# Performance work log

Measured on AMD Instinct MI355X. Metric: run time of the kernel, lower is better.

## Reference

```python
import jax, jax.numpy as jnp
import numpy as np

D_MODEL = 256
NUM_LAYERS = 4
NUM_FREQ = 16
D_STATE = 8
NUM_HEADS = 4
LN_EPS = 1e-5


def setup_inputs() -> dict:
    key = jax.random.key(0)
    ks = jax.random.split(key, 30)
    B, NS, NQ = 16, 1024, 1024
    D, L, S = D_MODEL, NUM_LAYERS, D_STATE
    cin = 2 * NUM_FREQ + 1  # 33
    w = lambda k, shp, s=0.02: jax.random.normal(k, shp, dtype=jnp.float32) * s
    inp = {
        'sparse_coords': jax.random.uniform(ks[0], (B, NS, 2), minval=-1.0, maxval=1.0, dtype=jnp.float32),
        'sparse_values': jax.random.normal(ks[1], (B, NS, 1), dtype=jnp.float32),
        'query_coords': jax.random.uniform(ks[2], (B, NQ, 2), minval=-1.0, maxval=1.0, dtype=jnp.float32),
        't': jax.random.uniform(ks[3], (B,), dtype=jnp.float32),
        'noise': jax.random.normal(ks[4], (B, NQ, 1), dtype=jnp.float32),
        'B_f': jax.random.normal(ks[5], (2, NUM_FREQ), dtype=jnp.float32) * 10.0,
        'Wq_in': w(ks[6], (D, cin)), 'bq_in': jnp.zeros((D,), jnp.float32),
        'Wi_in': w(ks[7], (D, cin)), 'bi_in': jnp.zeros((D,), jnp.float32),
        'A_log': jax.random.normal(ks[8], (L, S), dtype=jnp.float32) * 0.1 - 1.0,
        'Bw': w(ks[9], (L, S, D)),
        'Cw': w(ks[10], (L, D, S)),
        'Dp': jax.random.normal(ks[11], (L, D), dtype=jnp.float32) * 0.01,
        'ln_g': jnp.ones((L, D), jnp.float32), 'ln_b': jnp.zeros((L, D), jnp.float32),
        'gate_w': w(ks[12], (L, D, D)), 'gate_b': jnp.zeros((L, D), jnp.float32),
        'in_proj_w': w(ks[13], (3 * D, D)), 'in_proj_b': jnp.zeros((3 * D,), jnp.float32),
        'out_w': w(ks[14], (D, D)), 'out_b': jnp.zeros((D,), jnp.float32),
        'dec_w1': w(ks[15], (D, D)), 'dec_b1': jnp.zeros((D,), jnp.float32),
        'dec_w2': w(ks[16], (1, D)), 'dec_b2': jnp.zeros((1,), jnp.float32),
    }
    return inp


def _layernorm(x, g, b):
    mu = jnp.mean(x, axis=-1, keepdims=True)
    var = jnp.mean(jnp.square(x - mu), axis=-1, keepdims=True)
    return (x - mu) * jax.lax.rsqrt(var + LN_EPS) * g + b


def _ssm(x, A_log, Bw, Cw, Dp):
    # x: (B, N, D)
    Bsz, N, D = x.shape
    A = -jnp.clip(jnp.exp(A_log), 1e-8, 10.0)          # (S,)
    A_bar = jnp.exp(A / N)                              # dt = 1/N
    Bu = jnp.einsum('bnd,sd->bns', x, Bw)               # (B, N, S)

    def step(h, bu_t):
        h = A_bar * h + bu_t
        return h, h

    h0 = jnp.zeros((Bsz, A_log.shape[0]), x.dtype)
    _, hs = jax.lax.scan(step, h0, jnp.swapaxes(Bu, 0, 1))  # (N, B, S)
    hs = jnp.swapaxes(hs, 0, 1)                             # (B, N, S)
    return jnp.einsum('bns,ds->bnd', hs, Cw) + Dp * x


def _time_embed(t, dim):
    half = dim // 2
    freqs = jnp.exp(jnp.arange(half, dtype=jnp.float32) * (-jnp.log(10000.0) / (half - 1)))
    emb = t[:, None] * freqs[None, :]
    return jnp.concatenate([jnp.sin(emb), jnp.cos(emb)], axis=-1)


def _fourier(coords, B_f):
    proj = coords @ B_f
    return jnp.concatenate([jnp.sin(proj), jnp.cos(proj)], axis=-1)


def reference(sparse_coords, sparse_values, query_coords, t, noise, B_f,
              Wq_in, bq_in, Wi_in, bi_in,
              A_log, Bw, Cw, Dp, ln_g, ln_b, gate_w, gate_b,
              in_proj_w, in_proj_b, out_w, out_b,
              dec_w1, dec_b1, dec_w2, dec_b2):
    D = D_MODEL
    NS = sparse_coords.shape[1]
    sparse_feats = _fourier(sparse_coords, B_f)
    query_feats = _fourier(query_coords, B_f)
    input_tokens = jnp.concatenate([sparse_feats, sparse_values], -1) @ Wi_in.T + bi_in
    query_tokens = jnp.concatenate([query_feats, noise], -1) @ Wq_in.T + bq_in
    t_emb = _time_embed(t, D)[:, None, :]
    seq = jnp.concatenate([input_tokens + t_emb, query_tokens + t_emb], axis=1)

    for l in range(A_log.shape[0]):
        xn = _layernorm(seq, ln_g[l], ln_b[l])
        gate = jax.nn.sigmoid(xn @ gate_w[l].T + gate_b[l])
        seq = seq + gate * _ssm(xn, A_log[l], Bw[l], Cw[l], Dp[l])

    input_seq = seq[:, :NS, :]
    query_seq = seq[:, NS:, :]

    # multi-head cross-attention (torch nn.MultiheadAttention semantics)
    H, hd = NUM_HEADS, D // NUM_HEADS
    q = query_seq @ in_proj_w[:D].T + in_proj_b[:D]
    k = input_seq @ in_proj_w[D:2 * D].T + in_proj_b[D:2 * D]
    v = input_seq @ in_proj_w[2 * D:].T + in_proj_b[2 * D:]
    def split(x):
        b, n, _ = x.shape
        return x.reshape(b, n, H, hd).transpose(0, 2, 1, 3)
    q, k, v = split(q), split(k), split(v)
    scores = jnp.einsum('bhqd,bhkd->bhqk', q, k) / jnp.sqrt(jnp.float32(hd))
    attn = jax.nn.softmax(scores, axis=-1)
    o = jnp.einsum('bhqk,bhkd->bhqd', attn, v)
    o = o.transpose(0, 2, 1, 3).reshape(query_seq.shape[0], -1, D)
    attended = o @ out_w.T + out_b

    h = jax.nn.relu(attended @ dec_w1.T + dec_b1)
    return h @ dec_w2.T + dec_b2
```

## Files before the change

kernel.cpp:

```cpp
#include <hip/hip_runtime.h>
#include <math.h>


typedef float floatx4 __attribute__((ext_vector_type(4)));
typedef short shortx8 __attribute__((ext_vector_type(8)));

__device__ __forceinline__ unsigned short f2bf(float f) {
  unsigned u = __builtin_bit_cast(unsigned, f);
  u += 0x7FFFu + ((u >> 16) & 1u);
  return (unsigned short)(u >> 16);
}
__device__ __forceinline__ float bf2f(unsigned short h) {
  unsigned u = ((unsigned)h) << 16;
  return __builtin_bit_cast(float, u);
}
__device__ __forceinline__ unsigned cvt_pk_bf16(float a, float b) {
  unsigned r;
  asm("v_cvt_pk_bf16_f32 %0, %1, %2" : "=v"(r) : "v"(a), "v"(b));
  return r;
}
__device__ __forceinline__ void split2(float f0, float f1, unsigned& ph, unsigned& pl) {
  ph = cvt_pk_bf16(f0, f1);
  float r0 = f0 - __builtin_bit_cast(float, ph << 16);
  float r1 = f1 - __builtin_bit_cast(float, ph & 0xFFFF0000u);
  pl = cvt_pk_bf16(r0, r1);
}
__device__ __forceinline__ void split8(float4 a, float4 b, uint4& uh, uint4& ul) {
  unsigned h0, h1, h2, h3, l0, l1, l2, l3;
  split2(a.x, a.y, h0, l0);
  split2(a.z, a.w, h1, l1);
  split2(b.x, b.y, h2, l2);
  split2(b.z, b.w, h3, l3);
  uh = make_uint4(h0, h1, h2, h3);
  ul = make_uint4(l0, l1, l2, l3);
}
__device__ __forceinline__ shortx8 lds_frag(const unsigned short* S, int row, int u) {
  uint4 v = *(const uint4*)(S + row * 64 + ((u ^ (row & 7)) << 3));
  return __builtin_bit_cast(shortx8, v);
}
__device__ __forceinline__ shortx8 lds_frag_v(const unsigned short* S, int row, int u) {
  uint4 v = *(const uint4*)(S + row * 64 + (((u ^ row ^ (row >> 3)) & 7) << 3));
  return __builtin_bit_cast(shortx8, v);
}
__device__ __forceinline__ shortx8 gfrag(const unsigned short* p) {
  return __builtin_bit_cast(shortx8, *(const uint4*)p);
}
__device__ __forceinline__ floatx4 mfma16(shortx8 a, shortx8 b, floatx4 c) {
  return __builtin_amdgcn_mfma_f32_16x16x32_bf16(a, b, c, 0, 0, 0);
}
__device__ __forceinline__ float wave_sum64(float v) {
#pragma unroll
  for (int m = 1; m < 64; m <<= 1) v += __shfl_xor(v, m);
  return v;
}

__global__ __launch_bounds__(256) void wconv_k(
    const float* __restrict__ gw, const float* __restrict__ ipw,
    const float* __restrict__ ow, const float* __restrict__ d1w,
    unsigned short* __restrict__ dh, unsigned short* __restrict__ dl) {
  int i = (blockIdx.x * 256 + threadIdx.x) * 8;
  const float* src;
  if (i < 262144) src = gw + i;
  else if (i < 458752) src = ipw + (i - 262144);
  else if (i < 524288) src = ow + (i - 458752);
  else src = d1w + (i - 524288);
  uint4 uh, ul;
  split8(*(const float4*)src, *(const float4*)(src + 4), uh, ul);
  *(uint4*)(dh + i) = uh;
  *(uint4*)(dl + i) = ul;
}

__global__ __launch_bounds__(256) void wconv2_k(
    const float* __restrict__ Wi, const float* __restrict__ Wq,
    unsigned short* __restrict__ eh, unsigned short* __restrict__ el) {
  int idx = blockIdx.x * 256 + threadIdx.x;
  int sel = idx >> 14, rem = idx & 16383;
  int row = rem >> 6, k = rem & 63;
  float v = 0.f;
  if (k < 33) v = (sel ? Wq : Wi)[row * 33 + k];
  unsigned short h = f2bf(v);
  eh[idx] = h;
  el[idx] = f2bf(v - bf2f(h));
}

__global__ __launch_bounds__(256) void embed_k(
    const float* __restrict__ sc, const float* __restrict__ sv,
    const float* __restrict__ qc, const float* __restrict__ tarr,
    const float* __restrict__ noise, const float* __restrict__ Bf,
    const float* __restrict__ bq, const float* __restrict__ bi,
    const unsigned short* __restrict__ Weh, const unsigned short* __restrict__ Wel,
    float* __restrict__ seq) {
  __shared__ unsigned short Ah[64 * 64];
  __shared__ unsigned short Al[64 * 64];
  __shared__ float teb[256];
  int tid = threadIdx.x;
  int bid = blockIdx.x;
  int chunk = bid & 15, half = (bid >> 4) & 1, b = bid >> 5;
  int rowbase = b * 2048 + half * 1024 + chunk * 64;
  {
    uint4 z = make_uint4(0, 0, 0, 0);
    *(uint4*)(Ah + tid * 8) = z;
    *(uint4*)(Ah + 2048 + tid * 8) = z;
    *(uint4*)(Al + tid * 8) = z;
    *(uint4*)(Al + 2048 + tid * 8) = z;
  }
  {
    float t = tarr[b];
    int dd = tid & 127;
    float e = t * __expf((float)dd * -0.07252236513367074f);
    float v = (tid < 128) ? sinf(e) : cosf(e);
    teb[tid] = v + (half ? bq : bi)[tid];
  }
  __syncthreads();
  {
    int tok = tid >> 2;
    int n = chunk * 64 + tok;
    const float* cp = (half ? qc : sc) + (size_t)(b * 1024 + n) * 2;
    float cx = cp[0], cy = cp[1];
#pragma unroll
    for (int jj = 0; jj < 4; ++jj) {
      int fr = (tid & 3) * 4 + jj;
      float px = cx * Bf[fr] + cy * Bf[16 + fr];
      float s = sinf(px), c = cosf(px);
      unsigned short sh = f2bf(s), ch = f2bf(c);
      int ks = fr, kc = 16 + fr;
      Ah[tok * 64 + (((ks >> 3) ^ (tok & 7)) << 3) + (ks & 7)] = sh;
      Al[tok * 64 + (((ks >> 3) ^ (tok & 7)) << 3) + (ks & 7)] = f2bf(s - bf2f(sh));
      Ah[tok * 64 + (((kc >> 3) ^ (tok & 7)) << 3) + (kc & 7)] = ch;
      Al[tok * 64 + (((kc >> 3) ^ (tok & 7)) << 3) + (kc & 7)] = f2bf(c - bf2f(ch));
    }
    if ((tid & 3) == 0) {
      float vv = (half ? noise : sv)[b * 1024 + n];
      unsigned short vh = f2bf(vv);
      Ah[tok * 64 + ((4 ^ (tok & 7)) << 3)] = vh;
      Al[tok * 64 + ((4 ^ (tok & 7)) << 3)] = f2bf(vv - bf2f(vh));
    }
  }
  __syncthreads();
  int w = tid >> 6, lane = tid & 63, lm = lane & 15, quad = lane >> 4;
  const unsigned short* Wb = Weh + half * 16384;
  const unsigned short* Wbl = Wel + half * 16384;
  floatx4 acc[4][4] = {};
#pragma unroll
  for (int s = 0; s < 2; ++s) {
    shortx8 afh[4], afl[4];
#pragma unroll
    for (int i = 0; i < 4; ++i) {
      afh[i] = lds_frag(Ah, i * 16 + lm, s * 4 + quad);
      afl[i] = lds_frag(Al, i * 16 + lm, s * 4 + quad);
    }
#pragma unroll
    for (int n = 0; n < 4; ++n) {
      int wr = w * 64 + n * 16 + lm;
      shortx8 bh = gfrag(Wb + wr * 64 + (s * 4 + quad) * 8);
      shortx8 bl = gfrag(Wbl + wr * 64 + (s * 4 + quad) * 8);
#pragma unroll
      for (int i = 0; i < 4; ++i) {
        acc[i][n] = mfma16(afl[i], bh, acc[i][n]);
        acc[i][n] = mfma16(afh[i], bl, acc[i][n]);
        acc[i][n] = mfma16(afh[i], bh, acc[i][n]);
      }
    }
  }
#pragma unroll
  for (int i = 0; i < 4; ++i)
#pragma unroll
    for (int n = 0; n < 4; ++n) {
      int col = w * 64 + n * 16 + lm;
      float te = teb[col];
#pragma unroll
      for (int r = 0; r < 4; ++r) {
        int tok = i * 16 + quad * 4 + r;
        seq[(size_t)(rowbase + tok) * 256 + col] = acc[i][n][r] + te;
      }
    }
}

__global__ __launch_bounds__(256) void scan_k(
    const float* __restrict__ BuT, const float* __restrict__ A_log,
    float* __restrict__ hsT) {
  int tid = threadIdx.x;
  int wid = blockIdx.x * 4 + (tid >> 6);
  int lane = tid & 63;
  int b = wid >> 3, s = wid & 7;
  float A = -fminf(fmaxf(expf(A_log[s]), 1e-8f), 10.0f);
  float abar = expf(A * (1.0f / 2048.0f));
  size_t base = (size_t)s * 32768 + b * 2048 + lane * 32;
  const float4* bu4 = (const float4*)(BuT + base);
  float4 v[8];
#pragma unroll
  for (int k = 0; k < 8; ++k) v[k] = bu4[k];
  float bl = 0.f;
#pragma unroll
  for (int k = 0; k < 8; ++k) {
    bl = abar * bl + v[k].x;
    bl = abar * bl + v[k].y;
    bl = abar * bl + v[k].z;
    bl = abar * bl + v[k].w;
  }
  float a = expf(A * (32.0f / 2048.0f));
  float bb = bl;
#pragma unroll
  for (int off = 1; off < 64; off <<= 1) {
    float pa = __shfl_up(a, (unsigned)off);
    float pb = __shfl_up(bb, (unsigned)off);
    if (lane >= off) { bb = a * pb + bb; a = a * pa; }
  }
  float h = __shfl_up(bb, 1u);
  if (lane == 0) h = 0.f;
  float4* hp4 = (float4*)(hsT + base);
#pragma unroll
  for (int k = 0; k < 8; ++k) {
    float h0 = abar * h + v[k].x;
    float h1 = abar * h0 + v[k].y;
    float h2 = abar * h1 + v[k].z;
    float h3 = abar * h2 + v[k].w;
    hp4[k] = make_float4(h0, h1, h2, h3);
    h = h3;
  }
}

template <int HASUPD>
__global__ __launch_bounds__(256, 2) void pe_k(
    float* __restrict__ seq, const float* __restrict__ Gprev,
    const float* __restrict__ hsTp, const float* __restrict__ CwP,
    const float* __restrict__ DpP, const float* __restrict__ gP,
    const float* __restrict__ bP, const float* __restrict__ gC,
    const float* __restrict__ bC, const float* __restrict__ BwL,
    const unsigned short* __restrict__ Wh, const unsigned short* __restrict__ Wl,
    const float* __restrict__ gbias, float* __restrict__ Gout,
    float* __restrict__ BuT) {
  __shared__ unsigned short slab[64 * 536];
  __shared__ float hsL[8 * 64];
  __shared__ float BwLds[8 * 256];
  int tid = threadIdx.x;
  int m0 = (int)blockIdx.x * 64;
  int w = tid >> 6, lane = tid & 63, lm = lane & 15, quad = lane >> 4;

#pragma unroll
  for (int j = 0; j < 8; ++j) BwLds[j * 256 + tid] = BwL[j * 256 + tid];
  if (HASUPD) {
    hsL[tid] = hsTp[(size_t)(tid >> 6) * 32768 + m0 + (tid & 63)];
    int v1 = tid + 256;
    hsL[v1] = hsTp[(size_t)(v1 >> 6) * 32768 + m0 + (v1 & 63)];
  }

  if (HASUPD) {
    __syncthreads();
    int c0 = lane * 4;
    float cw[4][8], dp4[4];
#pragma unroll
    for (int n = 0; n < 4; ++n) {
      float4 a0 = *(const float4*)(CwP + (size_t)(c0 + n) * 8);
      float4 a1 = *(const float4*)(CwP + (size_t)(c0 + n) * 8 + 4);
      cw[n][0] = a0.x; cw[n][1] = a0.y; cw[n][2] = a0.z; cw[n][3] = a0.w;
      cw[n][4] = a1.x; cw[n][5] = a1.y; cw[n][6] = a1.z; cw[n][7] = a1.w;
      dp4[n] = DpP[c0 + n];
    }
    float4 gg = *(const float4*)(gP + c0);
    float4 bb = *(const float4*)(bP + c0);
#pragma unroll
    for (int rr = 0; rr < 16; ++rr) {
      int r = w * 16 + rr;
      int row = m0 + r;
      float4 x = *(const float4*)(seq + (size_t)row * 256 + c0);
      float s1 = x.x + x.y + x.z + x.w;
      float s2 = x.x * x.x + x.y * x.y + x.z * x.z + x.w * x.w;
#pragma unroll
      for (int mk = 1; mk < 64; mk <<= 1) {
        s1 += __shfl_xor(s1, mk);
        s2 += __shfl_xor(s2, mk);
      }
      float mu = s1 * (1.0f / 256.0f);
      float var = s2 * (1.0f / 256.0f) - mu * mu;
      float rs = rsqrtf(var + 1e-5f);
      float xn0 = (x.x - mu) * rs * gg.x + bb.x;
      float xn1 = (x.y - mu) * rs * gg.y + bb.y;
      float xn2 = (x.z - mu) * rs * gg.z + bb.z;
      float xn3 = (x.w - mu) * rs * gg.w + bb.w;
      float hv[8];
#pragma unroll
      for (int s = 0; s < 8; ++s) hv[s] = hsL[s * 64 + r];
      float y0 = dp4[0] * xn0, y1 = dp4[1] * xn1, y2 = dp4[2] * xn2, y3 = dp4[3] * xn3;
#pragma unroll
      for (int s = 0; s < 8; ++s) {
        y0 += hv[s] * cw[0][s];
        y1 += hv[s] * cw[1][s];
        y2 += hv[s] * cw[2][s];
        y3 += hv[s] * cw[3][s];
      }
      float4 gp = *(const float4*)(Gprev + (size_t)row * 256 + c0);
      x.x += gp.x * y0; x.y += gp.y * y1; x.z += gp.z * y2; x.w += gp.w * y3;
      *(float4*)(seq + (size_t)row * 256 + c0) = x;
      *(float4*)((char*)slab + (size_t)r * 1072 + c0 * 4) = x;
    }
    __syncthreads();
  }

  {
    int r = tid >> 2, q2 = tid & 3;
    int row = m0 + r;
    float4 xr[16];
#pragma unroll
    for (int j = 0; j < 16; ++j) {
      if (HASUPD)
        xr[j] = *(const float4*)((const char*)slab + (size_t)r * 1072 + (q2 * 64 + j * 4) * 4);
      else
        xr[j] = *(const float4*)(seq + (size_t)row * 256 + q2 * 64 + j * 4);
    }
    __syncthreads();
    float s1 = 0.f, s2 = 0.f;
#pragma unroll
    for (int j = 0; j < 16; ++j) {
      s1 += (xr[j].x + xr[j].y) + (xr[j].z + xr[j].w);
      s2 += (xr[j].x * xr[j].x + xr[j].y * xr[j].y) + (xr[j].z * xr[j].z + xr[j].w * xr[j].w);
    }
    s1 += __shfl_xor(s1, 1); s2 += __shfl_xor(s2, 1);
    s1 += __shfl_xor(s1, 2); s2 += __shfl_xor(s2, 2);
    float mu = s1 * (1.0f / 256.0f);
    float var = s2 * (1.0f / 256.0f) - mu * mu;
    float rs = rsqrtf(var + 1e-5f);
    float bu[8] = {};
#pragma unroll
    for (int j = 0; j < 16; ++j) {
      int c = q2 * 64 + j * 4;
      float4 gg = *(const float4*)(gC + c);
      float4 bb = *(const float4*)(bC + c);
      float4 xn;
      xn.x = (xr[j].x - mu) * rs * gg.x + bb.x;
      xn.y = (xr[j].y - mu) * rs * gg.y + bb.y;
      xn.z = (xr[j].z - mu) * rs * gg.z + bb.z;
      xn.w = (xr[j].w - mu) * rs * gg.w + bb.w;
#pragma unroll
      for (int s = 0; s < 8; ++s) {
        const float4 bw = *(const float4*)(BwLds + s * 256 + c);
        bu[s] += (xn.x * bw.x + xn.y * bw.y) + (xn.z * bw.z + xn.w * bw.w);
      }
      unsigned h0, l0, h1, l1;
      split2(xn.x, xn.y, h0, l0);
      split2(xn.z, xn.w, h1, l1);
      *(uint2*)((char*)slab + (size_t)r * 1072 + c * 2) = make_uint2(h0, h1);
      *(uint2*)((char*)slab + (size_t)r * 1072 + 512 + c * 2) = make_uint2(l0, l1);
    }
#pragma unroll
    for (int s = 0; s < 8; ++s) {
      bu[s] += __shfl_xor(bu[s], 1);
      bu[s] += __shfl_xor(bu[s], 2);
    }
    if (q2 == 0) {
#pragma unroll
      for (int s = 0; s < 8; ++s) BuT[(size_t)s * 32768 + row] = bu[s];
    }
  }
  __syncthreads();

  floatx4 acc[4][4] = {};
  {
    uint4 wa[8], wb[8];
    const size_t wcbase = (size_t)(w * 64 + lm) * 256 + quad * 8;
#pragma unroll
    for (int n = 0; n < 4; ++n) {
      wa[n * 2]     = *(const uint4*)(Wh + wcbase + (size_t)n * 16 * 256);
      wa[n * 2 + 1] = *(const uint4*)(Wl + wcbase + (size_t)n * 16 * 256);
    }
#pragma unroll
    for (int ku = 0; ku < 8; ++ku) {
      uint4* cur = (ku & 1) ? wb : wa;
      uint4* nxt = (ku & 1) ? wa : wb;
      if (ku < 7) {
        size_t koff = wcbase + (size_t)(ku + 1) * 32;
#pragma unroll
        for (int n = 0; n < 4; ++n) {
          nxt[n * 2]     = *(const uint4*)(Wh + koff + (size_t)n * 16 * 256);
          nxt[n * 2 + 1] = *(const uint4*)(Wl + koff + (size_t)n * 16 * 256);
        }
      }
      int slot = ku * 4 + quad;
      shortx8 afh[4], afl[4];
#pragma unroll
      for (int m = 0; m < 4; ++m) {
        const char* rb = (const char*)slab + (size_t)(m * 16 + lm) * 1072;
        afh[m] = __builtin_bit_cast(shortx8, *(const uint4*)(rb + slot * 16));
        afl[m] = __builtin_bit_cast(shortx8, *(const uint4*)(rb + 512 + slot * 16));
      }
#pragma unroll
      for (int m = 0; m < 4; ++m)
#pragma unroll
        for (int n = 0; n < 4; ++n) {
          shortx8 bh = __builtin_bit_cast(shortx8, cur[n * 2]);
          shortx8 bl = __builtin_bit_cast(shortx8, cur[n * 2 + 1]);
          acc[m][n] = mfma16(afl[m], bh, acc[m][n]);
          acc[m][n] = mfma16(afh[m], bl, acc[m][n]);
          acc[m][n] = mfma16(afh[m], bh, acc[m][n]);
        }
    }
  }
  float bi4[4];
#pragma unroll
  for (int n = 0; n < 4; ++n) bi4[n] = gbias[w * 64 + n * 16 + lm];
#pragma unroll
  for (int m = 0; m < 4; ++m)
#pragma unroll
    for (int r = 0; r < 4; ++r) {
      int row = m0 + m * 16 + quad * 4 + r;
#pragma unroll
      for (int n = 0; n < 4; ++n) {
        int col = w * 64 + n * 16 + lm;
        float v = acc[m][n][r] + bi4[n];
        Gout[(size_t)row * 256 + col] = 1.0f / (1.0f + __expf(-v));
      }
    }
}

__global__ __launch_bounds__(256) void upd_k(
    float* __restrict__ seq, const float* __restrict__ G,
    const float* __restrict__ hsT, const float* __restrict__ Cw,
    const float* __restrict__ Dp, const float* __restrict__ g,
    const float* __restrict__ be) {
  int tid = threadIdx.x;
  int row = blockIdx.x * 4 + (tid >> 6);
  int lane = tid & 63;
  int c0 = lane * 4;
  float4 x = *(const float4*)(seq + (size_t)row * 256 + c0);
  float s1 = x.x + x.y + x.z + x.w;
  float s2 = x.x * x.x + x.y * x.y + x.z * x.z + x.w * x.w;
#pragma unroll
  for (int mk = 1; mk < 64; mk <<= 1) {
    s1 += __shfl_xor(s1, mk);
    s2 += __shfl_xor(s2, mk);
  }
  float mu = s1 * (1.0f / 256.0f);
  float var = s2 * (1.0f / 256.0f) - mu * mu;
  float rs = rsqrtf(var + 1e-5f);
  float4 gg = *(const float4*)(g + c0);
  float4 bb = *(const float4*)(be + c0);
  float xn0 = (x.x - mu) * rs * gg.x + bb.x;
  float xn1 = (x.y - mu) * rs * gg.y + bb.y;
  float xn2 = (x.z - mu) * rs * gg.z + bb.z;
  float xn3 = (x.w - mu) * rs * gg.w + bb.w;
  float hv[8];
#pragma unroll
  for (int s = 0; s < 8; ++s) hv[s] = hsT[(size_t)s * 32768 + row];
  float y0, y1, y2, y3;
  {
    float4 d = *(const float4*)(Dp + c0);
    y0 = d.x * xn0; y1 = d.y * xn1; y2 = d.z * xn2; y3 = d.w * xn3;
  }
#pragma unroll
  for (int n = 0; n < 4; ++n) {
    float4 a0 = *(const float4*)(Cw + (size_t)(c0 + n) * 8);
    float4 a1 = *(const float4*)(Cw + (size_t)(c0 + n) * 8 + 4);
    float yn = hv[0] * a0.x + hv[1] * a0.y + hv[2] * a0.z + hv[3] * a0.w +
               hv[4] * a1.x + hv[5] * a1.y + hv[6] * a1.z + hv[7] * a1.w;
    if (n == 0) y0 += yn;
    else if (n == 1) y1 += yn;
    else if (n == 2) y2 += yn;
    else y3 += yn;
  }
  float4 gp = *(const float4*)(G + (size_t)row * 256 + c0);
  x.x += gp.x * y0; x.y += gp.y * y1; x.z += gp.z * y2; x.w += gp.w * y3;
  *(float4*)(seq + (size_t)row * 256 + c0) = x;
}

template <int MODE, int ASPLIT>
__global__ __launch_bounds__(256, 4) void mgemm_k(
    const void* __restrict__ Aptr, const unsigned short* __restrict__ Alp,
    const unsigned short* __restrict__ Wh, const unsigned short* __restrict__ Wl,
    const float* __restrict__ bias, void* __restrict__ C0, void* __restrict__ C1,
    int ldc, int aClog, int aStride, int aBase, int gxlog) {
  __shared__ unsigned short Ash[64 * 64];
  __shared__ unsigned short Asl[64 * 64];
  __shared__ unsigned short Bsh[64 * 72];
  __shared__ unsigned short Bsl[64 * 72];
  int tid = threadIdx.x;
  int nwg = (int)gridDim.x;
  int vbid = ((blockIdx.x & 7) * (nwg >> 3)) + (blockIdx.x >> 3);
  int bx = vbid & ((1 << gxlog) - 1);
  int by = vbid >> gxlog;
  int n0 = bx * 64, m0 = by * 64;
  int w = tid >> 6, lane = tid & 63;
  int wm = w & 1, wn = w >> 1;
  int lm = lane & 15, quad = lane >> 4;
  int sr2 = tid >> 2, q2 = tid & 3;
  unsigned aMask = (1u << aClog) - 1u;
  int am = m0 + sr2;
  int garow = ((am >> aClog) * aStride) + aBase + (int)((unsigned)am & aMask);
  int wrow = n0 + sr2;
  uint4 ah[2], al[2], wh4[2], wl4[2];
  auto load_chunk = [&](int kc) {
    if (ASPLIT) {
      const unsigned short* pa =
          (const unsigned short*)Aptr + (size_t)garow * 256 + kc * 64 + q2 * 8;
      ah[0] = *(const uint4*)pa;
      ah[1] = *(const uint4*)(pa + 32);
      const unsigned short* pl = Alp + (pa - (const unsigned short*)Aptr);
      al[0] = *(const uint4*)pl;
      al[1] = *(const uint4*)(pl + 32);
    } else {
      const float* pa = (const float*)Aptr + (size_t)garow * 256 + kc * 64 + q2 * 8;
      split8(*(const float4*)pa, *(const float4*)(pa + 4), ah[0], al[0]);
      split8(*(const float4*)(pa + 32), *(const float4*)(pa + 36), ah[1], al[1]);
    }
    const unsigned short* pw = Wh + (size_t)wrow * 256 + kc * 64 + q2 * 8;
    wh4[0] = *(const uint4*)pw;
    wh4[1] = *(const uint4*)(pw + 32);
    const unsigned short* pwl = Wl + (pw - Wh);
    wl4[0] = *(const uint4*)pwl;
    wl4[1] = *(const uint4*)(pwl + 32);
  };
  int kc0 = (bx + 1) & 3;
  load_chunk(kc0);
  floatx4 acc[2][2] = {};
  for (int j = 0; j < 4; ++j) {
    __syncthreads();
    {
      int off0 = sr2 * 64 + ((q2 ^ (sr2 & 7)) << 3);
      int off1 = sr2 * 64 + (((q2 + 4) ^ (sr2 & 7)) << 3);
      *(uint4*)(Ash + off0) = ah[0];
      *(uint4*)(Ash + off1) = ah[1];
      *(uint4*)(Asl + off0) = al[0];
      *(uint4*)(Asl + off1) = al[1];
      *(uint4*)(Bsh + off0) = wh4[0];
      *(uint4*)(Bsh + off1) = wh4[1];
      *(uint4*)(Bsl + off0) = wl4[0];
      *(uint4*)(Bsl + off1) = wl4[1];
    }
    __syncthreads();
    if (j < 3) load_chunk((kc0 + j + 1) & 3);
#pragma unroll
    for (int s = 0; s < 2; ++s) {
      int u = s * 4 + quad;
      shortx8 afh[2], afl[2], bfh[2], bfl[2];
#pragma unroll
      for (int i = 0; i < 2; ++i) {
        int rr = wm * 32 + i * 16 + lm;
        afh[i] = lds_frag(Ash, rr, u);
        afl[i] = lds_frag(Asl, rr, u);
        int rc = wn * 32 + i * 16 + lm;
        bfh[i] = lds_frag(Bsh, rc, u);
        bfl[i] = lds_frag(Bsl, rc, u);
      }
#pragma unroll
      for (int i = 0; i < 2; ++i)
#pragma unroll
        for (int n = 0; n < 2; ++n) {
          acc[i][n] = mfma16(afl[i], bfh[n], acc[i][n]);
          acc[i][n] = mfma16(afh[i], bfl[n], acc[i][n]);
          acc[i][n] = mfma16(afh[i], bfh[n], acc[i][n]);
        }
    }
  }
  if (MODE == 3) {
    unsigned short* Ch = (unsigned short*)C0;
    unsigned short* Cl = (unsigned short*)C1;
    float bi4[2];
#pragma unroll
    for (int n = 0; n < 2; ++n) bi4[n] = bias[n0 + wn * 32 + n * 16 + lm];
    __syncthreads();
#pragma unroll
    for (int i = 0; i < 2; ++i)
#pragma unroll
      for (int r = 0; r < 4; ++r) {
        int rr = wm * 32 + i * 16 + quad * 4 + r;
        int c0i = wn * 32 + lm;
        float vA = acc[i][0][r] + bi4[0];
        float vB = acc[i][1][r] + bi4[1];
        unsigned ph, pl;
        split2(vA, vB, ph, pl);
        Bsh[rr * 72 + c0i] = (unsigned short)ph;
        Bsh[rr * 72 + c0i + 16] = (unsigned short)(ph >> 16);
        Bsl[rr * 72 + c0i] = (unsigned short)pl;
        Bsl[rr * 72 + c0i + 16] = (unsigned short)(pl >> 16);
      }
    __syncthreads();
#pragma unroll
    for (int f = 0; f < 2; ++f) {
      int row = (tid >> 3) + f * 32;
      int slot = tid & 7;
      size_t go = (size_t)(m0 + row) * ldc + n0 + slot * 8;
      *(uint4*)(Ch + go) = *(const uint4*)(Bsh + row * 72 + slot * 8);
      *(uint4*)(Cl + go) = *(const uint4*)(Bsl + row * 72 + slot * 8);
    }
  } else {
    float* Cf = (float*)C0;
#pragma unroll
    for (int i = 0; i < 2; ++i)
#pragma unroll
      for (int r = 0; r < 4; ++r) {
        int row = m0 + wm * 32 + i * 16 + quad * 4 + r;
#pragma unroll
        for (int n = 0; n < 2; ++n) {
          int col = n0 + wn * 32 + n * 16 + lm;
          float v = acc[i][n][r] + bias[col];
          if (MODE == 1) v = fmaxf(v, 0.0f);
          Cf[(size_t)row * ldc + col] = v;
        }
      }
  }
}

__global__ __launch_bounds__(256, 2) void attn_k(
    const unsigned short* __restrict__ qh, const unsigned short* __restrict__ ql,
    const unsigned short* __restrict__ kvh, const unsigned short* __restrict__ kvl,
    float* __restrict__ ob) {
  __shared__ unsigned short Ksh[2][64 * 64];
  __shared__ unsigned short Ksl[2][64 * 64];
  __shared__ unsigned short Vt[2][64 * 64];
  __shared__ unsigned short Ps[4 * 16 * 64];
  int tid = threadIdx.x;
  int bid = blockIdx.x;
  int bh = bid & 63, qt = bid >> 6;
  int h = bh & 3, b = bh >> 2;
  int w = tid >> 6, lane = tid & 63, lm = lane & 15, quad = lane >> 4;
  int sr = tid >> 3, scu = tid & 7;
  unsigned short* Pw = Ps + w * 1024;
  shortx8 qfh[2], qfl[2];
  {
    size_t qoff = (size_t)(b * 1024 + qt * 64 + w * 16 + lm) * 256 + h * 64;
#pragma unroll
    for (int s = 0; s < 2; ++s) {
      qfh[s] = gfrag(qh + qoff + s * 32 + quad * 8);
      qfl[s] = gfrag(ql + qoff + s * 32 + quad * 8);
    }
  }
  float lac = 0.f;
  floatx4 oacc[4] = {};
  const size_t kvbase = ((size_t)(b * 1024)) * 512 + h * 64;
  const float sc_l2 = 0.125f * 1.44269504089f;
  int vg = tid & 7, vk = (tid >> 3) * 2;
  uint4 kh4[2], kl4[2], vv0, vv1;
  auto load_kv = [&](int kt) {
#pragma unroll
    for (int p = 0; p < 2; ++p) {
      int r = sr + p * 32;
      size_t a = kvbase + (size_t)(kt * 64 + r) * 512 + scu * 8;
      kh4[p] = *(const uint4*)(kvh + a);
      kl4[p] = *(const uint4*)(kvl + a);
    }
    vv0 = *(const uint4*)(kvh + kvbase + (size_t)(kt * 64 + vk) * 512 + 256 + vg * 8);
    vv1 = *(const uint4*)(kvh + kvbase + (size_t)(kt * 64 + vk + 1) * 512 + 256 + vg * 8);
  };
  const int kt0 = qt & 15;
  load_kv(kt0);
  for (int it = 0; it < 16; ++it) {
    int cur = it & 1;
    unsigned short* KshC = Ksh[cur];
    unsigned short* KslC = Ksl[cur];
    unsigned short* VtC = Vt[cur];
#pragma unroll
    for (int p = 0; p < 2; ++p) {
      int r = sr + p * 32;
      int off = r * 64 + ((scu ^ (r & 7)) << 3);
      *(uint4*)(KshC + off) = kh4[p];
      *(uint4*)(KslC + off) = kl4[p];
    }
    {
      shortx8 s0 = __builtin_bit_cast(shortx8, vv0);
      shortx8 s1 = __builtin_bit_cast(shortx8, vv1);
      unsigned short* vb = VtC + vg * 512 + (vk & 7);
      int x0 = ((vk >> 3) ^ vg) & 7;
#pragma unroll
      for (int j = 0; j < 8; ++j) {
        unsigned pack = ((unsigned)(unsigned short)s0[j]) |
                        (((unsigned)(unsigned short)s1[j]) << 16);
        *(unsigned*)(vb + j * 64 + ((x0 ^ j) << 3)) = pack;
      }
    }
    __syncthreads();
    if (it < 15) load_kv((kt0 + it + 1) & 15);
    floatx4 sacc[4] = {};
#pragma unroll
    for (int s = 0; s < 2; ++s) {
#pragma unroll
      for (int m = 0; m < 4; ++m) {
        shortx8 kfh = lds_frag(KshC, m * 16 + lm, s * 4 + quad);
        shortx8 kfl = lds_frag(KslC, m * 16 + lm, s * 4 + quad);
        sacc[m] = mfma16(kfl, qfh[s], sacc[m]);
        sacc[m] = mfma16(kfh, qfl[s], sacc[m]);
        sacc[m] = mfma16(kfh, qfh[s], sacc[m]);
      }
    }
#pragma unroll
    for (int m = 0; m < 4; ++m) {
      float p0 = exp2f(sacc[m][0] * sc_l2 - 12.0f);
      float p1 = exp2f(sacc[m][1] * sc_l2 - 12.0f);
      float p2 = exp2f(sacc[m][2] * sc_l2 - 12.0f);
      float p3 = exp2f(sacc[m][3] * sc_l2 - 12.0f);
      lac += (p0 + p1) + (p2 + p3);
      int u = (m * 2 + (quad >> 1)) ^ (lm & 7);
      unsigned short* base = Pw + lm * 64 + u * 8 + (quad & 1) * 4;
      *(uint2*)base = make_uint2(cvt_pk_bf16(p0, p1), cvt_pk_bf16(p2, p3));
    }
#pragma unroll
    for (int s = 0; s < 2; ++s) {
      shortx8 pf = lds_frag(Pw, lm, s * 4 + quad);
#pragma unroll
      for (int n = 0; n < 4; ++n) {
        shortx8 vf = lds_frag_v(VtC, n * 16 + lm, s * 4 + quad);
        oacc[n] = mfma16(pf, vf, oacc[n]);
      }
    }
  }
  lac += __shfl_xor(lac, 16);
  lac += __shfl_xor(lac, 32);
  const size_t obase = ((size_t)(b * 1024 + qt * 64 + w * 16)) * 256 + h * 64;
#pragma unroll
  for (int r = 0; r < 4; ++r) {
    int row = quad * 4 + r;
    float inv = 1.0f / __shfl(lac, row);
#pragma unroll
    for (int n = 0; n < 4; ++n)
      ob[obase + (size_t)row * 256 + n * 16 + lm] = oacc[n][r] * inv;
  }
}

__global__ __launch_bounds__(256) void dec2_k(const float* __restrict__ hb,
                                              const float* __restrict__ w2,
                                              const float* __restrict__ b2,
                                              float* __restrict__ out) {
  int tid = threadIdx.x;
  int m = blockIdx.x * 4 + (tid >> 6);
  int lane = tid & 63;
  float4 h4 = *(const float4*)(hb + (size_t)m * 256 + lane * 4);
  float4 w4 = *(const float4*)(w2 + lane * 4);
  float v = h4.x * w4.x + h4.y * w4.y + h4.z * w4.z + h4.w * w4.w;
  v = wave_sum64(v);
  if (lane == 0) out[m] = v + b2[0];
}

extern "C" void kernel_launch(void* const* d_in, const int* in_sizes, int n_in,
                              void* d_out, int out_size, void* d_ws, size_t ws_size,
                              hipStream_t stream) {
  const float* sparse_coords = (const float*)d_in[0];
  const float* sparse_values = (const float*)d_in[1];
  const float* query_coords  = (const float*)d_in[2];
  const float* t_arr         = (const float*)d_in[3];
  const float* noise         = (const float*)d_in[4];
  const float* B_f           = (const float*)d_in[5];
  const float* Wq_in         = (const float*)d_in[6];
  const float* bq_in         = (const float*)d_in[7];
  const float* Wi_in         = (const float*)d_in[8];
  const float* bi_in         = (const float*)d_in[9];
  const float* A_log         = (const float*)d_in[10];
  const float* Bw            = (const float*)d_in[11];
  const float* Cw            = (const float*)d_in[12];
  const float* Dp            = (const float*)d_in[13];
  const float* ln_g          = (const float*)d_in[14];
  const float* ln_b          = (const float*)d_in[15];
  const float* gate_w        = (const float*)d_in[16];
  const float* gate_b        = (const float*)d_in[17];
  const float* in_proj_w     = (const float*)d_in[18];
  const float* in_proj_b     = (const float*)d_in[19];
  const float* out_w         = (const float*)d_in[20];
  const float* out_b         = (const float*)d_in[21];
  const float* dec_w1        = (const float*)d_in[22];
  const float* dec_b1        = (const float*)d_in[23];
  const float* dec_w2        = (const float*)d_in[24];
  const float* dec_b2        = (const float*)d_in[25];

  unsigned short* us = (unsigned short*)d_ws;
  float* seq = (float*)us;
  float* G = (float*)(us + 16777216);
  unsigned short* qhp = us + 33554432;
  unsigned short* qlp = qhp + 4194304;
  unsigned short* kvh = qlp + 4194304;
  unsigned short* kvl = kvh + 8388608;
  float* BuT = (float*)(kvl + 8388608);
  float* hsT = BuT + 262144;
  unsigned short* whi = (unsigned short*)(hsT + 262144);
  unsigned short* wlo = whi + 589824;
  unsigned short* Weh = wlo + 589824;
  unsigned short* Wel = Weh + 32768;
  float* obuf = G;
  float* attb = (float*)qhp;
  float* hrel = (float*)kvh;

  wconv_k<<<288, 256, 0, stream>>>(gate_w, in_proj_w, out_w, dec_w1, whi, wlo);
  wconv2_k<<<128, 256, 0, stream>>>(Wi_in, Wq_in, Weh, Wel);
  embed_k<<<512, 256, 0, stream>>>(sparse_coords, sparse_values, query_coords,
                                   t_arr, noise, B_f, bq_in, bi_in, Weh, Wel, seq);
  pe_k<0><<<512, 256, 0, stream>>>(seq, nullptr, nullptr, nullptr, nullptr,
                                   nullptr, nullptr, ln_g, ln_b, Bw,
                                   whi, wlo, gate_b, G, BuT);
  scan_k<<<32, 256, 0, stream>>>(BuT, A_log, hsT);
  for (int l = 1; l < 4; ++l) {
    pe_k<1><<<512, 256, 0, stream>>>(
        seq, G, hsT, Cw + (l - 1) * 2048, Dp + (l - 1) * 256,
        ln_g + (l - 1) * 256, ln_b + (l - 1) * 256,
        ln_g + l * 256, ln_b + l * 256, Bw + l * 2048,
        whi + l * 65536, wlo + l * 65536, gate_b + l * 256, G, BuT);
    scan_k<<<32, 256, 0, stream>>>(BuT, A_log + l * 8, hsT);
  }
  upd_k<<<8192, 256, 0, stream>>>(seq, G, hsT, Cw + 3 * 2048, Dp + 3 * 256,
                                  ln_g + 768, ln_b + 768);
  mgemm_k<3, 0><<<1024, 256, 0, stream>>>(
      seq, nullptr, whi + 262144, wlo + 262144, in_proj_b, qhp, qlp,
      256, 10, 2048, 1024, 2);
  mgemm_k<3, 0><<<2048, 256, 0, stream>>>(
      seq, nullptr, whi + 327680, wlo + 327680, in_proj_b + 256, kvh, kvl,
      512, 10, 2048, 0, 3);
  attn_k<<<1024, 256, 0, stream>>>(qhp, qlp, kvh, kvl, obuf);
  mgemm_k<0, 0><<<1024, 256, 0, stream>>>(
      obuf, nullptr, whi + 458752, wlo + 458752, out_b, attb, nullptr,
      256, 30, 0, 0, 2);
  mgemm_k<1, 0><<<1024, 256, 0, stream>>>(
      attb, nullptr, whi + 524288, wlo + 524288, dec_b1, hrel, nullptr,
      256, 30, 0, 0, 2);
  dec2_k<<<4096, 256, 0, stream>>>(hrel, dec_w2, dec_b2, (float*)d_out);
}
```

Measured before the change: 543.0 us.

## Restructure projection GEMMs as row-slab kernels and fuse decoder chain

Replaces the tiled 64x64 split-bf16 GEMM with row-slab kernels. Each block splits a 32-row fp32 slab into hi/lo bf16 in LDS once, and each wave streams its weight columns straight from global memory with register double-buffering, so there is no per-k-chunk LDS staging of weights. The out-projection, first decoder layer with ReLU and final dot product are fused into one kernel, keeping intermediates in LDS and dropping two intermediate global round-trips and two launches. The cost is fewer, larger blocks at lower occupancy and weights re-read from global/L2 by every block.

```diff
diff --git a/kernel.cpp b/kernel.cpp
--- a/kernel.cpp
+++ b/kernel.cpp
@@ -462,141 +462,266 @@
   *(float4*)(seq + (size_t)row * 256 + c0) = x;
 }
 
-template <int MODE, int ASPLIT>
-__global__ __launch_bounds__(256, 4) void mgemm_k(
-    const void* __restrict__ Aptr, const unsigned short* __restrict__ Alp,
-    const unsigned short* __restrict__ Wh, const unsigned short* __restrict__ Wl,
-    const float* __restrict__ bias, void* __restrict__ C0, void* __restrict__ C1,
-    int ldc, int aClog, int aStride, int aBase, int gxlog) {
-  __shared__ unsigned short Ash[64 * 64];
-  __shared__ unsigned short Asl[64 * 64];
-  __shared__ unsigned short Bsh[64 * 72];
-  __shared__ unsigned short Bsl[64 * 72];
+template <int NPASS>
+__global__ __launch_bounds__(256, 2) void proj_k(
+    const float* __restrict__ src, const unsigned short* __restrict__ Wh,
+    const unsigned short* __restrict__ Wl, const float* __restrict__ bias,
+    unsigned short* __restrict__ Ch, unsigned short* __restrict__ Cl,
+    int ldc, int aBase) {
+  __shared__ unsigned short slab[32 * 536];
   int tid = threadIdx.x;
-  int nwg = (int)gridDim.x;
-  int vbid = ((blockIdx.x & 7) * (nwg >> 3)) + (blockIdx.x >> 3);
-  int bx = vbid & ((1 << gxlog) - 1);
-  int by = vbid >> gxlog;
-  int n0 = bx * 64, m0 = by * 64;
-  int w = tid >> 6, lane = tid & 63;
-  int wm = w & 1, wn = w >> 1;
-  int lm = lane & 15, quad = lane >> 4;
-  int sr2 = tid >> 2, q2 = tid & 3;
-  unsigned aMask = (1u << aClog) - 1u;
-  int am = m0 + sr2;
-  int garow = ((am >> aClog) * aStride) + aBase + (int)((unsigned)am & aMask);
-  int wrow = n0 + sr2;
-  uint4 ah[2], al[2], wh4[2], wl4[2];
-  auto load_chunk = [&](int kc) {
-    if (ASPLIT) {
-      const unsigned short* pa =
-          (const unsigned short*)Aptr + (size_t)garow * 256 + kc * 64 + q2 * 8;
-      ah[0] = *(const uint4*)pa;
-      ah[1] = *(const uint4*)(pa + 32);
-      const unsigned short* pl = Alp + (pa - (const unsigned short*)Aptr);
-      al[0] = *(const uint4*)pl;
-      al[1] = *(const uint4*)(pl + 32);
-    } else {
-      const float* pa = (const float*)Aptr + (size_t)garow * 256 + kc * 64 + q2 * 8;
-      split8(*(const float4*)pa, *(const float4*)(pa + 4), ah[0], al[0]);
-      split8(*(const float4*)(pa + 32), *(const float4*)(pa + 36), ah[1], al[1]);
-    }
-    const unsigned short* pw = Wh + (size_t)wrow * 256 + kc * 64 + q2 * 8;
-    wh4[0] = *(const uint4*)pw;
-    wh4[1] = *(const uint4*)(pw + 32);
-    const unsigned short* pwl = Wl + (pw - Wh);
-    wl4[0] = *(const uint4*)pwl;
-    wl4[1] = *(const uint4*)(pwl + 32);
-  };
-  int kc0 = (bx + 1) & 3;
-  load_chunk(kc0);
-  floatx4 acc[2][2] = {};
-  for (int j = 0; j < 4; ++j) {
-    __syncthreads();
+  int m0 = (int)blockIdx.x * 32;
+  int w = tid >> 6, lane = tid & 63, lm = lane & 15, quad = lane >> 4;
+  {
+    int r = tid >> 3, q8 = tid & 7;
+    int am = m0 + r;
+    int garow = ((am >> 10) * 2048) + aBase + (am & 1023);
+    const float* sp = src + (size_t)garow * 256 + q8 * 32;
+    char* rb = (char*)slab + (size_t)r * 1072;
+#pragma unroll
+    for (int j = 0; j < 8; ++j) {
+      float4 x = *(const float4*)(sp + j * 4);
+      unsigned h0, l0, h1, l1;
+      split2(x.x, x.y, h0, l0);
+      split2(x.z, x.w, h1, l1);
+      int c = q8 * 32 + j * 4;
+      *(uint2*)(rb + c * 2) = make_uint2(h0, h1);
+      *(uint2*)(rb + 512 + c * 2) = make_uint2(l0, l1);
+    }
+  }
+  __syncthreads();
+#pragma unroll
+  for (int cp = 0; cp < NPASS; ++cp) {
+    floatx4 acc[2][4] = {};
     {
-      int off0 = sr2 * 64 + ((q2 ^ (sr2 & 7)) << 3);
-      int off1 = sr2 * 64 + (((q2 + 4) ^ (sr2 & 7)) << 3);
-      *(uint4*)(Ash + off0) = ah[0];
-      *(uint4*)(Ash + off1) = ah[1];
-      *(uint4*)(Asl + off0) = al[0];
-      *(uint4*)(Asl + off1) = al[1];
-      *(uint4*)(Bsh + off0) = wh4[0];
-      *(uint4*)(Bsh + off1) = wh4[1];
-      *(uint4*)(Bsl + off0) = wl4[0];
-      *(uint4*)(Bsl + off1) = wl4[1];
-    }
-    __syncthreads();
-    if (j < 3) load_chunk((kc0 + j + 1) & 3);
-#pragma unroll
-    for (int s = 0; s < 2; ++s) {
-      int u = s * 4 + quad;
-      shortx8 afh[2], afl[2], bfh[2], bfl[2];
-#pragma unroll
-      for (int i = 0; i < 2; ++i) {
-        int rr = wm * 32 + i * 16 + lm;
-        afh[i] = lds_frag(Ash, rr, u);
-        afl[i] = lds_frag(Asl, rr, u);
-        int rc = wn * 32 + i * 16 + lm;
-        bfh[i] = lds_frag(Bsh, rc, u);
-        bfl[i] = lds_frag(Bsl, rc, u);
-      }
-#pragma unroll
-      for (int i = 0; i < 2; ++i)
-#pragma unroll
-        for (int n = 0; n < 2; ++n) {
-          acc[i][n] = mfma16(afl[i], bfh[n], acc[i][n]);
-          acc[i][n] = mfma16(afh[i], bfl[n], acc[i][n]);
-          acc[i][n] = mfma16(afh[i], bfh[n], acc[i][n]);
-        }
-    }
-  }
-  if (MODE == 3) {
-    unsigned short* Ch = (unsigned short*)C0;
-    unsigned short* Cl = (unsigned short*)C1;
-    float bi4[2];
-#pragma unroll
-    for (int n = 0; n < 2; ++n) bi4[n] = bias[n0 + wn * 32 + n * 16 + lm];
-    __syncthreads();
-#pragma unroll
-    for (int i = 0; i < 2; ++i)
+      uint4 wa[8], wb[8];
+      const size_t wcbase = (size_t)(cp * 256 + w * 64 + lm) * 256 + quad * 8;
+#pragma unroll
+      for (int n = 0; n < 4; ++n) {
+        wa[n * 2]     = *(const uint4*)(Wh + wcbase + (size_t)n * 16 * 256);
+        wa[n * 2 + 1] = *(const uint4*)(Wl + wcbase + (size_t)n * 16 * 256);
+      }
+#pragma unroll
+      for (int ku = 0; ku < 8; ++ku) {
+        uint4* cur = (ku & 1) ? wb : wa;
+        uint4* nxt = (ku & 1) ? wa : wb;
+        if (ku < 7) {
+          size_t koff = wcbase + (size_t)(ku + 1) * 32;
+#pragma unroll
+          for (int n = 0; n < 4; ++n) {
+            nxt[n * 2]     = *(const uint4*)(Wh + koff + (size_t)n * 16 * 256);
+            nxt[n * 2 + 1] = *(const uint4*)(Wl + koff + (size_t)n * 16 * 256);
+          }
+        }
+        int slot = ku * 4 + quad;
+        shortx8 afh[2], afl[2];
+#pragma unroll
+        for (int m = 0; m < 2; ++m) {
+          const char* rb = (const char*)slab + (size_t)(m * 16 + lm) * 1072;
+          afh[m] = __builtin_bit_cast(shortx8, *(const uint4*)(rb + slot * 16));
+          afl[m] = __builtin_bit_cast(shortx8, *(const uint4*)(rb + 512 + slot * 16));
+        }
+#pragma unroll
+        for (int m = 0; m < 2; ++m)
+#pragma unroll
+          for (int n = 0; n < 4; ++n) {
+            shortx8 bh = __builtin_bit_cast(shortx8, cur[n * 2]);
+            shortx8 bl = __builtin_bit_cast(shortx8, cur[n * 2 + 1]);
+            acc[m][n] = mfma16(afl[m], bh, acc[m][n]);
+            acc[m][n] = mfma16(afh[m], bl, acc[m][n]);
+            acc[m][n] = mfma16(afh[m], bh, acc[m][n]);
+          }
+      }
+    }
+    float bi4[4];
+#pragma unroll
+    for (int n = 0; n < 4; ++n) bi4[n] = bias[cp * 256 + w * 64 + n * 16 + lm];
+#pragma unroll
+    for (int m = 0; m < 2; ++m)
 #pragma unroll
       for (int r = 0; r < 4; ++r) {
-        int rr = wm * 32 + i * 16 + quad * 4 + r;
-        int c0i = wn * 32 + lm;
-        float vA = acc[i][0][r] + bi4[0];
-        float vB = acc[i][1][r] + bi4[1];
-        unsigned ph, pl;
-        split2(vA, vB, ph, pl);
-        Bsh[rr * 72 + c0i] = (unsigned short)ph;
-        Bsh[rr * 72 + c0i + 16] = (unsigned short)(ph >> 16);
-        Bsl[rr * 72 + c0i] = (unsigned short)pl;
-        Bsl[rr * 72 + c0i + 16] = (unsigned short)(pl >> 16);
-      }
-    __syncthreads();
-#pragma unroll
-    for (int f = 0; f < 2; ++f) {
-      int row = (tid >> 3) + f * 32;
-      int slot = tid & 7;
-      size_t go = (size_t)(m0 + row) * ldc + n0 + slot * 8;
-      *(uint4*)(Ch + go) = *(const uint4*)(Bsh + row * 72 + slot * 8);
-      *(uint4*)(Cl + go) = *(const uint4*)(Bsl + row * 72 + slot * 8);
-    }
-  } else {
-    float* Cf = (float*)C0;
-#pragma unroll
-    for (int i = 0; i < 2; ++i)
+        int row = m0 + m * 16 + quad * 4 + r;
+        size_t ro = (size_t)row * ldc + cp * 256;
+#pragma unroll
+        for (int np = 0; np < 2; ++np) {
+          int colA = w * 64 + (2 * np) * 16 + lm;
+          float vA = acc[m][2 * np][r] + bi4[2 * np];
+          float vB = acc[m][2 * np + 1][r] + bi4[2 * np + 1];
+          unsigned ph, pl;
+          split2(vA, vB, ph, pl);
+          Ch[ro + colA] = (unsigned short)ph;
+          Ch[ro + colA + 16] = (unsigned short)(ph >> 16);
+          Cl[ro + colA] = (unsigned short)pl;
+          Cl[ro + colA + 16] = (unsigned short)(pl >> 16);
+        }
+      }
+  }
+}
+
+__global__ __launch_bounds__(256, 2) void dec_k(
+    const float* __restrict__ src, const unsigned short* __restrict__ W1h,
+    const unsigned short* __restrict__ W1l, const float* __restrict__ b1,
+    const unsigned short* __restrict__ W2h, const unsigned short* __restrict__ W2l,
+    const float* __restrict__ b2v, const float* __restrict__ w2,
+    const float* __restrict__ b2, float* __restrict__ out) {
+  __shared__ unsigned short slab[32 * 536];
+  __shared__ float pw[4][32];
+  int tid = threadIdx.x;
+  int m0 = (int)blockIdx.x * 32;
+  int w = tid >> 6, lane = tid & 63, lm = lane & 15, quad = lane >> 4;
+  {
+    int r = tid >> 3, q8 = tid & 7;
+    const float* sp = src + (size_t)(m0 + r) * 256 + q8 * 32;
+    char* rb = (char*)slab + (size_t)r * 1072;
+#pragma unroll
+    for (int j = 0; j < 8; ++j) {
+      float4 x = *(const float4*)(sp + j * 4);
+      unsigned h0, l0, h1, l1;
+      split2(x.x, x.y, h0, l0);
+      split2(x.z, x.w, h1, l1);
+      int c = q8 * 32 + j * 4;
+      *(uint2*)(rb + c * 2) = make_uint2(h0, h1);
+      *(uint2*)(rb + 512 + c * 2) = make_uint2(l0, l1);
+    }
+  }
+  __syncthreads();
+  floatx4 acc[2][4] = {};
+  {
+    uint4 wa[8], wb[8];
+    const size_t wcbase = (size_t)(w * 64 + lm) * 256 + quad * 8;
+#pragma unroll
+    for (int n = 0; n < 4; ++n) {
+      wa[n * 2]     = *(const uint4*)(W1h + wcbase + (size_t)n * 16 * 256);
+      wa[n * 2 + 1] = *(const uint4*)(W1l + wcbase + (size_t)n * 16 * 256);
+    }
+#pragma unroll
+    for (int ku = 0; ku < 8; ++ku) {
+      uint4* cur = (ku & 1) ? wb : wa;
+      uint4* nxt = (ku & 1) ? wa : wb;
+      if (ku < 7) {
+        size_t koff = wcbase + (size_t)(ku + 1) * 32;
+#pragma unroll
+        for (int n = 0; n < 4; ++n) {
+          nxt[n * 2]     = *(const uint4*)(W1h + koff + (size_t)n * 16 * 256);
+          nxt[n * 2 + 1] = *(const uint4*)(W1l + koff + (size_t)n * 16 * 256);
+        }
+      }
+      int slot = ku * 4 + quad;
+      shortx8 afh[2], afl[2];
+#pragma unroll
+      for (int m = 0; m < 2; ++m) {
+        const char* rb = (const char*)slab + (size_t)(m * 16 + lm) * 1072;
+        afh[m] = __builtin_bit_cast(shortx8, *(const uint4*)(rb + slot * 16));
+        afl[m] = __builtin_bit_cast(shortx8, *(const uint4*)(rb + 512 + slot * 16));
+      }
+#pragma unroll
+      for (int m = 0; m < 2; ++m)
+#pragma unroll
+        for (int n = 0; n < 4; ++n) {
+          shortx8 bh = __builtin_bit_cast(shortx8, cur[n * 2]);
+          shortx8 bl = __builtin_bit_cast(shortx8, cur[n * 2 + 1]);
+          acc[m][n] = mfma16(afl[m], bh, acc[m][n]);
+          acc[m][n] = mfma16(afh[m], bl, acc[m][n]);
+          acc[m][n] = mfma16(afh[m], bh, acc[m][n]);
+        }
+    }
+  }
+  __syncthreads();
+  {
+    float bi4[4];
+#pragma unroll
+    for (int n = 0; n < 4; ++n) bi4[n] = b1[w * 64 + n * 16 + lm];
+#pragma unroll
+    for (int m = 0; m < 2; ++m)
 #pragma unroll
       for (int r = 0; r < 4; ++r) {
-        int row = m0 + wm * 32 + i * 16 + quad * 4 + r;
-#pragma unroll
-        for (int n = 0; n < 2; ++n) {
-          int col = n0 + wn * 32 + n * 16 + lm;
-          float v = acc[i][n][r] + bias[col];
-          if (MODE == 1) v = fmaxf(v, 0.0f);
-          Cf[(size_t)row * ldc + col] = v;
-        }
-      }
-  }
+        int rr = m * 16 + quad * 4 + r;
+        char* rb = (char*)slab + (size_t)rr * 1072;
+#pragma unroll
+        for (int np = 0; np < 2; ++np) {
+          int cA = w * 64 + (2 * np) * 16 + lm;
+          int cB = cA + 16;
+          float vA = acc[m][2 * np][r] + bi4[2 * np];
+          float vB = acc[m][2 * np + 1][r] + bi4[2 * np + 1];
+          unsigned ph, pl;
+          split2(vA, vB, ph, pl);
+          *(unsigned short*)(rb + cA * 2) = (unsigned short)ph;
+          *(unsigned short*)(rb + cB * 2) = (unsigned short)(ph >> 16);
+          *(unsigned short*)(rb + 512 + cA * 2) = (unsigned short)pl;
+          *(unsigned short*)(rb + 512 + cB * 2) = (unsigned short)(pl >> 16);
+        }
+      }
+  }
+  __syncthreads();
+  floatx4 acc2[2][4] = {};
+  {
+    uint4 wa[8], wb[8];
+    const size_t wcbase = (size_t)(w * 64 + lm) * 256 + quad * 8;
+#pragma unroll
+    for (int n = 0; n < 4; ++n) {
+      wa[n * 2]     = *(const uint4*)(W2h + wcbase + (size_t)n * 16 * 256);
+      wa[n * 2 + 1] = *(const uint4*)(W2l + wcbase + (size_t)n * 16 * 256);
+    }
+#pragma unroll
+    for (int ku = 0; ku < 8; ++ku) {
+      uint4* cur = (ku & 1) ? wb : wa;
+      uint4* nxt = (ku & 1) ? wa : wb;
+      if (ku < 7) {
+        size_t koff = wcbase + (size_t)(ku + 1) * 32;
+#pragma unroll
+        for (int n = 0; n < 4; ++n) {
+          nxt[n * 2]     = *(const uint4*)(W2h + koff + (size_t)n * 16 * 256);
+          nxt[n * 2 + 1] = *(const uint4*)(W2l + koff + (size_t)n * 16 * 256);
+        }
+      }
+      int slot = ku * 4 + quad;
+      shortx8 afh[2], afl[2];
+#pragma unroll
+      for (int m = 0; m < 2; ++m) {
+        const char* rb = (const char*)slab + (size_t)(m * 16 + lm) * 1072;
+        afh[m] = __builtin_bit_cast(shortx8, *(const uint4*)(rb + slot * 16));
+        afl[m] = __builtin_bit_cast(shortx8, *(const uint4*)(rb + 512 + slot * 16));
+      }
+#pragma unroll
+      for (int m = 0; m < 2; ++m)
+#pragma unroll
+        for (int n = 0; n < 4; ++n) {
+          shortx8 bh = __builtin_bit_cast(shortx8, cur[n * 2]);
+          shortx8 bl = __builtin_bit_cast(shortx8, cur[n * 2 + 1]);
+          acc2[m][n] = mfma16(afl[m], bh, acc2[m][n]);
+          acc2[m][n] = mfma16(afh[m], bl, acc2[m][n]);
+          acc2[m][n] = mfma16(afh[m], bh, acc2[m][n]);
+        }
+    }
+  }
+  {
+    float b14[4], w24[4];
+#pragma unroll
+    for (int n = 0; n < 4; ++n) {
+      int col = w * 64 + n * 16 + lm;
+      b14[n] = b2v[col];
+      w24[n] = w2[col];
+    }
+#pragma unroll
+    for (int m = 0; m < 2; ++m)
+#pragma unroll
+      for (int r = 0; r < 4; ++r) {
+        float p = 0.f;
+#pragma unroll
+        for (int n = 0; n < 4; ++n) {
+          float hvv = fmaxf(acc2[m][n][r] + b14[n], 0.0f);
+          p += hvv * w24[n];
+        }
+        p += __shfl_xor(p, 1);
+        p += __shfl_xor(p, 2);
+        p += __shfl_xor(p, 4);
+        p += __shfl_xor(p, 8);
+        if (lm == 0) pw[w][m * 16 + quad * 4 + r] = p;
+      }
+  }
+  __syncthreads();
+  if (tid < 32)
+    out[m0 + tid] = pw[0][tid] + pw[1][tid] + pw[2][tid] + pw[3][tid] + b2[0];
 }
 
 __global__ __launch_bounds__(256, 2) void attn_k(
@@ -712,20 +837,6 @@
     for (int n = 0; n < 4; ++n)
       ob[obase + (size_t)row * 256 + n * 16 + lm] = oacc[n][r] * inv;
   }
-}
-
-__global__ __launch_bounds__(256) void dec2_k(const float* __restrict__ hb,
-                                              const float* __restrict__ w2,
-                                              const float* __restrict__ b2,
-                                              float* __restrict__ out) {
-  int tid = threadIdx.x;
-  int m = blockIdx.x * 4 + (tid >> 6);
-  int lane = tid & 63;
-  float4 h4 = *(const float4*)(hb + (size_t)m * 256 + lane * 4);
-  float4 w4 = *(const float4*)(w2 + lane * 4);
-  float v = h4.x * w4.x + h4.y * w4.y + h4.z * w4.z + h4.w * w4.w;
-  v = wave_sum64(v);
-  if (lane == 0) out[m] = v + b2[0];
 }
 
 extern "C" void kernel_launch(void* const* d_in, const int* in_sizes, int n_in,
@@ -772,8 +883,6 @@
   unsigned short* Weh = wlo + 589824;
   unsigned short* Wel = Weh + 32768;
   float* obuf = G;
-  float* attb = (float*)qhp;
-  float* hrel = (float*)kvh;
 
   wconv_k<<<288, 256, 0, stream>>>(gate_w, in_proj_w, out_w, dec_w1, whi, wlo);
   wconv2_k<<<128, 256, 0, stream>>>(Wi_in, Wq_in, Weh, Wel);
@@ -793,18 +902,12 @@
   }
   upd_k<<<8192, 256, 0, stream>>>(seq, G, hsT, Cw + 3 * 2048, Dp + 3 * 256,
                                   ln_g + 768, ln_b + 768);
-  mgemm_k<3, 0><<<1024, 256, 0, stream>>>(
-      seq, nullptr, whi + 262144, wlo + 262144, in_proj_b, qhp, qlp,
-      256, 10, 2048, 1024, 2);
-  mgemm_k<3, 0><<<2048, 256, 0, stream>>>(
-      seq, nullptr, whi + 327680, wlo + 327680, in_proj_b + 256, kvh, kvl,
-      512, 10, 2048, 0, 3);
+  proj_k<1><<<512, 256, 0, stream>>>(seq, whi + 262144, wlo + 262144,
+                                     in_proj_b, qhp, qlp, 256, 1024);
+  proj_k<2><<<512, 256, 0, stream>>>(seq, whi + 327680, wlo + 327680,
+                                     in_proj_b + 256, kvh, kvl, 512, 0);
   attn_k<<<1024, 256, 0, stream>>>(qhp, qlp, kvh, kvl, obuf);
-  mgemm_k<0, 0><<<1024, 256, 0, stream>>>(
-      obuf, nullptr, whi + 458752, wlo + 458752, out_b, attb, nullptr,
-      256, 30, 0, 0, 2);
-  mgemm_k<1, 0><<<1024, 256, 0, stream>>>(
-      attb, nullptr, whi + 524288, wlo + 524288, dec_b1, hrel, nullptr,
-      256, 30, 0, 0, 2);
-  dec2_k<<<4096, 256, 0, stream>>>(hrel, dec_w2, dec_b2, (float*)d_out);
-}
+  dec_k<<<512, 256, 0, stream>>>(obuf, whi + 458752, wlo + 458752, out_b,
+                                 whi + 524288, wlo + 524288, dec_b1, dec_w2,
+                                 dec_b2, (float*)d_out);
+}
```

Result: faster. 513.5 us (-5.4%).
